# Optimization experiments

Hardware: AMD Instinct MI355X
Metric: run time of the kernel (lower is better)

The kernel has to match this reference:

```python
import jax, jax.numpy as jnp
import numpy as np

N = 100_000          # NEURON_COUNT (scaled)
INPUT_SIZE = 1024    # input neurons occupy indices [0, INPUT_SIZE)
OUTPUT_SIZE = 256    # output neurons occupy indices [N-OUTPUT_SIZE, N)
E = 10_000_000       # SYNAPSE_RATIO * N
STEPS = 3


def setup_inputs() -> dict:
    key = jax.random.key(0)
    k1, k2, k3, k4, k5 = jax.random.split(key, 5)
    x = jax.random.normal(k1, (INPUT_SIZE,), dtype=jnp.float32)
    synapse_weights = jax.random.normal(k2, (E,), dtype=jnp.float32)
    neuron_biases = jax.random.normal(k3, (N - INPUT_SIZE,), dtype=jnp.float32)
    synapse_src = jax.random.randint(k4, (E,), 0, N, dtype=jnp.int64) if jax.config.jax_enable_x64 else jax.random.randint(k4, (E,), 0, N, dtype=jnp.int32)
    synapse_dst = jax.random.randint(k5, (E,), 0, N, dtype=jnp.int64) if jax.config.jax_enable_x64 else jax.random.randint(k5, (E,), 0, N, dtype=jnp.int32)
    return {
        "x": x,
        "synapse_weights": synapse_weights,
        "neuron_biases": neuron_biases,
        "synapse_src": synapse_src,
        "synapse_dst": synapse_dst,
    }


def reference(x, synapse_weights, neuron_biases, synapse_src, synapse_dst):
    # Initial state: zeros everywhere, inputs injected at the first INPUT_SIZE slots.
    v = jnp.zeros((N,), dtype=x.dtype).at[:INPUT_SIZE].set(x.reshape(-1))
    # tanh applied to all neurons except outputs (last OUTPUT_SIZE indices)
    tanh_mask = jnp.arange(N) < (N - OUTPUT_SIZE)
    for _ in range(STEPS):
        # vectorized gather-multiply-scatter: next[to] += v[from] * w  (one segment_sum)
        msg = v[synapse_src] * synapse_weights                       # [E]
        nxt = jax.ops.segment_sum(msg, synapse_dst, num_segments=N)  # [N]
        # biases added to all non-input neurons
        nxt = nxt.at[INPUT_SIZE:].add(neuron_biases)
        # tanh everywhere except output neurons
        v = jnp.where(tanh_mask, jnp.tanh(nxt), nxt)
    return v[N - OUTPUT_SIZE:]
```

## Files before the change

### kernel.cpp

```cpp
#include <hip/hip_runtime.h>

#define N_NEURONS   100000
#define INPUT_SIZE  1024
#define OUTPUT_SIZE 256
#define E_SYN       10000000
#define STEPS       3

#define RANGES      8
#define BIN         12500
#define SCAT_BLK    512
#define CBLK        96
#define CAP         1280000
#define RB_BLK      256
#define CH          5000
#define B_CNT       2000
#define VEC4        (E_SYN / 4)

__global__ void init_all(const float* __restrict__ x, float* __restrict__ v,
                         int* __restrict__ gcur) {
    int i = blockIdx.x * blockDim.x + threadIdx.x;
    if (i < N_NEURONS) v[i] = (i < INPUT_SIZE) ? x[i] : 0.0f;
    if (i < RANGES) gcur[i] = 0;
}

__global__ void reorder_partition(const float* __restrict__ w,
                                  const int*   __restrict__ src,
                                  const int*   __restrict__ dst,
                                  int2* __restrict__ recs,
                                  int*  __restrict__ gcur) {
    __shared__ int cnt[RANGES];
    __shared__ int cursor[RANGES];
    const int tid  = threadIdx.x;
    const int lane = tid & 63;
    const unsigned long long ltmask = (1ull << lane) - 1ull;
    if (tid < RANGES) cnt[tid] = 0;
    __syncthreads();

    const int beg  = blockIdx.x * CH;
    const int endx = beg + CH;
    const int ITER = (CH + RB_BLK - 1) / RB_BLK;

    int wcnt = 0;
    for (int it = 0; it < ITER; ++it) {
        int  e  = beg + it * RB_BLK + tid;
        bool ok = (e < endx);
        int  r  = ok ? (dst[e] / BIN) : -1;
#pragma unroll
        for (int rr = 0; rr < RANGES; ++rr) {
            unsigned long long mask = __ballot(r == rr);
            if (lane == rr) wcnt += __popcll(mask);
        }
    }
    if (lane < RANGES) atomicAdd(&cnt[lane], wcnt);
    __syncthreads();
    if (tid < RANGES) cursor[tid] = tid * CAP + atomicAdd(&gcur[tid], cnt[tid]);
    __syncthreads();

    for (int it = 0; it < ITER; ++it) {
        int  e  = beg + it * RB_BLK + tid;
        bool ok = (e < endx);
        int  d  = ok ? dst[e] : 0;
        int  r  = ok ? (d / BIN) : -1;
        int  pos = 0;
#pragma unroll
        for (int rr = 0; rr < RANGES; ++rr) {
            unsigned long long mask = __ballot(r == rr);
            int tot = __popcll(mask);
            int b = 0;
            if (lane == rr) b = atomicAdd(&cursor[rr], tot);
            b = __shfl(b, rr, 64);
            if (r == rr) pos = b + __popcll(mask & ltmask);
        }
        if (ok) {
            int code = (src[e] << 14) | (d - r * BIN);
            recs[pos] = make_int2(code, __float_as_int(w[e]));
        }
    }
}

__global__ __launch_bounds__(SCAT_BLK) void scatter_sorted(
        const int2* __restrict__ recs,
        const int*  __restrict__ gcur,
        const float* __restrict__ v,
        float* __restrict__ partials) {
    __shared__ float bins[BIN];
    const int r = blockIdx.x / CBLK;
    const int c = blockIdx.x % CBLK;
    for (int j = threadIdx.x; j < BIN; j += SCAT_BLK) bins[j] = 0.0f;
    __syncthreads();

    const int cnt   = gcur[r];
    const int npair = cnt >> 1;
    const int4* base4 = (const int4*)(recs + (size_t)r * CAP);
    const int stride = CBLK * SCAT_BLK;
    for (int u = c * SCAT_BLK + threadIdx.x; u < npair; u += stride) {
        int4 p = base4[u];
        atomicAdd(&bins[p.x & 16383], v[p.x >> 14] * __int_as_float(p.y));
        atomicAdd(&bins[p.z & 16383], v[p.z >> 14] * __int_as_float(p.w));
    }
    if ((cnt & 1) && c == 0 && threadIdx.x == 0) {
        int2 p = recs[(size_t)r * CAP + cnt - 1];
        atomicAdd(&bins[p.x & 16383], v[p.x >> 14] * __int_as_float(p.y));
    }
    __syncthreads();
    float* o = partials + (size_t)(r * CBLK + c) * BIN;
    for (int j = threadIdx.x; j < BIN; j += SCAT_BLK) o[j] = bins[j];
}

__global__ void reduce_update(const float* __restrict__ partials,
                              const float* __restrict__ bias,
                              float* __restrict__ v,
                              float* __restrict__ out,
                              int C, int write_out) {
    int i4 = 4 * (blockIdx.x * blockDim.x + threadIdx.x);
    if (i4 >= N_NEURONS) return;
    const int r = i4 / BIN;
    const int j = i4 - r * BIN;
    const float* base = partials + ((size_t)r * C) * BIN + j;
    float4 acc = {0.f, 0.f, 0.f, 0.f};
    for (int c = 0; c < C; ++c) {
        float4 p = *(const float4*)(base + (size_t)c * BIN);
        acc.x += p.x; acc.y += p.y; acc.z += p.z; acc.w += p.w;
    }
    float av[4] = {acc.x, acc.y, acc.z, acc.w};
#pragma unroll
    for (int k = 0; k < 4; ++k) {
        int i = i4 + k;
        float val = av[k] + ((i >= INPUT_SIZE) ? bias[i - INPUT_SIZE] : 0.0f);
        float nv  = (i < N_NEURONS - OUTPUT_SIZE) ? tanhf(val) : val;
        v[i] = nv;
        if (write_out && i >= N_NEURONS - OUTPUT_SIZE)
            out[i - (N_NEURONS - OUTPUT_SIZE)] = val;
    }
}

__global__ void init_state_fb(const float* __restrict__ x, float* __restrict__ v) {
    int i = blockIdx.x * blockDim.x + threadIdx.x;
    if (i < N_NEURONS) v[i] = (i < INPUT_SIZE) ? x[i] : 0.0f;
}
__global__ void scatter_binned(const float* __restrict__ w,
                               const int*   __restrict__ src,
                               const int*   __restrict__ dst,
                               const float* __restrict__ v,
                               float*       __restrict__ partials,
                               int C) {
    __shared__ float bins[BIN];
    const int r = blockIdx.x / C;
    const int c = blockIdx.x % C;
    const int lo = r * BIN;
    const int hi = lo + BIN;
    for (int j = threadIdx.x; j < BIN; j += blockDim.x) bins[j] = 0.0f;
    __syncthreads();
    const int4*   src4 = (const int4*)src;
    const int4*   dst4 = (const int4*)dst;
    const float4* w4v  = (const float4*)w;
    const int stride = C * blockDim.x;
    for (int u = c * blockDim.x + threadIdx.x; u < VEC4; u += stride) {
        const int4   s4 = src4[u];
        const int4   d4 = dst4[u];
        const float4 wv = w4v[u];
        int   s[4] = {s4.x, s4.y, s4.z, s4.w};
        int   d[4] = {d4.x, d4.y, d4.z, d4.w};
        float ww[4] = {wv.x, wv.y, wv.z, wv.w};
#pragma unroll
        for (int k = 0; k < 4; ++k)
            if (d[k] >= lo && d[k] < hi)
                atomicAdd(&bins[d[k] - lo], v[s[k]] * ww[k]);
    }
    __syncthreads();
    float* o = partials + ((size_t)(r * C + c)) * BIN;
    for (int j = threadIdx.x; j < BIN; j += blockDim.x) o[j] = bins[j];
}

extern "C" void kernel_launch(void* const* d_in, const int* in_sizes, int n_in,
                              void* d_out, int out_size, void* d_ws, size_t ws_size,
                              hipStream_t stream) {
    const float* x    = (const float*)d_in[0];
    const float* w    = (const float*)d_in[1];
    const float* bias = (const float*)d_in[2];
    const int*   src  = (const int*)d_in[3];
    const int*   dst  = (const int*)d_in[4];
    float* out = (float*)d_out;

    const int blk = 256;
    const int grid_n   = (N_NEURONS + blk - 1) / blk;
    const int red_grid = (N_NEURONS / 4 + blk - 1) / blk;

    float* v        = (float*)d_ws;
    float* partials = v + N_NEURONS;
    int2*  recs     = (int2*)(partials + (size_t)RANGES * CBLK * BIN);
    int*   gcur     = (int*)(recs + (size_t)RANGES * CAP);
    size_t need = (size_t)((char*)(gcur + RANGES) - (char*)d_ws);

    if (ws_size >= need) {
        init_all<<<grid_n, blk, 0, stream>>>(x, v, gcur);
        reorder_partition<<<B_CNT, RB_BLK, 0, stream>>>(w, src, dst, recs, gcur);
        for (int s = 0; s < STEPS; ++s) {
            scatter_sorted<<<RANGES * CBLK, SCAT_BLK, 0, stream>>>(
                recs, gcur, v, partials);
            reduce_update<<<red_grid, blk, 0, stream>>>(
                partials, bias, v, out, CBLK, s == STEPS - 1 ? 1 : 0);
        }
    } else {
        long C = (long)(ws_size / 4 / N_NEURONS) - 1;
        if (C > 64) C = 64;
        if (C < 1) C = 1;
        float* part_fb = v + N_NEURONS;
        init_state_fb<<<grid_n, blk, 0, stream>>>(x, v);
        for (int s = 0; s < STEPS; ++s) {
            scatter_binned<<<RANGES * (int)C, SCAT_BLK, 0, stream>>>(
                w, src, dst, v, part_fb, (int)C);
            reduce_update<<<red_grid, blk, 0, stream>>>(
                part_fb, bias, v, out, (int)C, s == STEPS - 1 ? 1 : 0);
        }
    }
}
```

Measured before the change: 461.1 us.

## Speed up partition with ballot bit-planes, unroll scatter, split reduction into two stages

```diff
diff --git a/kernel.cpp b/kernel.cpp
--- a/kernel.cpp
+++ b/kernel.cpp
@@ -10,10 +10,12 @@
 #define BIN         12500
 #define SCAT_BLK    512
 #define CBLK        96
+#define RG          8
+#define RSL         (CBLK / RG)
 #define CAP         1280000
 #define RB_BLK      256
-#define CH          5000
-#define B_CNT       2000
+#define CH          4000
+#define B_CNT       2500
 #define VEC4        (E_SYN / 4)
 
 __global__ void init_all(const float* __restrict__ x, float* __restrict__ v,
@@ -23,15 +25,18 @@
     if (i < RANGES) gcur[i] = 0;
 }
 
-__global__ void reorder_partition(const float* __restrict__ w,
-                                  const int*   __restrict__ src,
-                                  const int*   __restrict__ dst,
-                                  int2* __restrict__ recs,
-                                  int*  __restrict__ gcur) {
+__global__ __launch_bounds__(RB_BLK) void reorder_partition(
+        const float* __restrict__ w,
+        const int*   __restrict__ src,
+        const int*   __restrict__ dst,
+        int2* __restrict__ recs,
+        int*  __restrict__ gcur) {
     __shared__ int cnt[RANGES];
     __shared__ int cursor[RANGES];
+    __shared__ int wbase[RB_BLK / 64][RANGES];
     const int tid  = threadIdx.x;
     const int lane = tid & 63;
+    const int wv   = tid >> 6;
     const unsigned long long ltmask = (1ull << lane) - 1ull;
     if (tid < RANGES) cnt[tid] = 0;
     __syncthreads();
@@ -39,42 +44,59 @@
     const int beg  = blockIdx.x * CH;
     const int endx = beg + CH;
     const int ITER = (CH + RB_BLK - 1) / RB_BLK;
-
-    int wcnt = 0;
-    for (int it = 0; it < ITER; ++it) {
-        int  e  = beg + it * RB_BLK + tid;
-        bool ok = (e < endx);
-        int  r  = ok ? (dst[e] / BIN) : -1;
-#pragma unroll
-        for (int rr = 0; rr < RANGES; ++rr) {
-            unsigned long long mask = __ballot(r == rr);
-            if (lane == rr) wcnt += __popcll(mask);
-        }
-    }
-    if (lane < RANGES) atomicAdd(&cnt[lane], wcnt);
-    __syncthreads();
-    if (tid < RANGES) cursor[tid] = tid * CAP + atomicAdd(&gcur[tid], cnt[tid]);
-    __syncthreads();
-
+    const int* wi  = (const int*)w;
+
+    int h[RANGES] = {0, 0, 0, 0, 0, 0, 0, 0};
     for (int it = 0; it < ITER; ++it) {
         int  e  = beg + it * RB_BLK + tid;
         bool ok = (e < endx);
         int  d  = ok ? dst[e] : 0;
-        int  r  = ok ? (d / BIN) : -1;
-        int  pos = 0;
+        int  r  = d / BIN;
+        unsigned long long okm = __ballot(ok);
+        unsigned long long b0  = __ballot(r & 1);
+        unsigned long long b1  = __ballot(r & 2);
+        unsigned long long b2  = __ballot(r & 4);
 #pragma unroll
         for (int rr = 0; rr < RANGES; ++rr) {
-            unsigned long long mask = __ballot(r == rr);
-            int tot = __popcll(mask);
-            int b = 0;
-            if (lane == rr) b = atomicAdd(&cursor[rr], tot);
-            b = __shfl(b, rr, 64);
-            if (r == rr) pos = b + __popcll(mask & ltmask);
+            unsigned long long m = ((rr & 1) ? b0 : ~b0) &
+                                   ((rr & 2) ? b1 : ~b1) &
+                                   ((rr & 4) ? b2 : ~b2) & okm;
+            h[rr] += __popcll(m);
         }
-        if (ok) {
-            int code = (src[e] << 14) | (d - r * BIN);
-            recs[pos] = make_int2(code, __float_as_int(w[e]));
-        }
+    }
+    if (lane < RANGES) {
+        int t = h[0];
+#pragma unroll
+        for (int rr = 1; rr < RANGES; ++rr) if (lane == rr) t = h[rr];
+        atomicAdd(&cnt[lane], t);
+    }
+    __syncthreads();
+    if (tid < RANGES) cursor[tid] = tid * CAP + atomicAdd(&gcur[tid], cnt[tid]);
+    __syncthreads();
+
+    for (int it = 0; it < ITER; ++it) {
+        int  e  = beg + it * RB_BLK + tid;
+        bool ok = (e < endx);
+        int  d  = ok ? dst[e] : 0;
+        int  sv = ok ? src[e] : 0;
+        int  wb = ok ? wi[e]  : 0;
+        int  r  = d / BIN;
+        unsigned long long okm = __ballot(ok);
+        unsigned long long b0  = __ballot(r & 1);
+        unsigned long long b1  = __ballot(r & 2);
+        unsigned long long b2  = __ballot(r & 4);
+        unsigned long long s0 = (lane & 1) ? b0 : ~b0;
+        unsigned long long s1 = (lane & 2) ? b1 : ~b1;
+        unsigned long long s2 = (lane & 4) ? b2 : ~b2;
+        int tot = __popcll(s0 & s1 & s2 & okm);
+        if (lane < RANGES) wbase[wv][lane] = atomicAdd(&cursor[lane], tot);
+        unsigned long long m0 = (r & 1) ? b0 : ~b0;
+        unsigned long long m1 = (r & 2) ? b1 : ~b1;
+        unsigned long long m2 = (r & 4) ? b2 : ~b2;
+        unsigned long long mym = m0 & m1 & m2 & okm;
+        int base = wbase[wv][r];
+        int pos  = base + __popcll(mym & ltmask);
+        if (ok) recs[pos] = make_int2((sv << 14) | (d - r * BIN), wb);
     }
 }
 
@@ -93,10 +115,23 @@
     const int npair = cnt >> 1;
     const int4* base4 = (const int4*)(recs + (size_t)r * CAP);
     const int stride = CBLK * SCAT_BLK;
-    for (int u = c * SCAT_BLK + threadIdx.x; u < npair; u += stride) {
-        int4 p = base4[u];
-        atomicAdd(&bins[p.x & 16383], v[p.x >> 14] * __int_as_float(p.y));
-        atomicAdd(&bins[p.z & 16383], v[p.z >> 14] * __int_as_float(p.w));
+    int u = c * SCAT_BLK + threadIdx.x;
+    for (; u + stride < npair; u += 2 * stride) {
+        int4 a = base4[u];
+        int4 b = base4[u + stride];
+        float va0 = v[a.x >> 14];
+        float va1 = v[a.z >> 14];
+        float vb0 = v[b.x >> 14];
+        float vb1 = v[b.z >> 14];
+        atomicAdd(&bins[a.x & 16383], va0 * __int_as_float(a.y));
+        atomicAdd(&bins[a.z & 16383], va1 * __int_as_float(a.w));
+        atomicAdd(&bins[b.x & 16383], vb0 * __int_as_float(b.y));
+        atomicAdd(&bins[b.z & 16383], vb1 * __int_as_float(b.w));
+    }
+    if (u < npair) {
+        int4 a = base4[u];
+        atomicAdd(&bins[a.x & 16383], v[a.x >> 14] * __int_as_float(a.y));
+        atomicAdd(&bins[a.z & 16383], v[a.z >> 14] * __int_as_float(a.w));
     }
     if ((cnt & 1) && c == 0 && threadIdx.x == 0) {
         int2 p = recs[(size_t)r * CAP + cnt - 1];
@@ -107,19 +142,34 @@
     for (int j = threadIdx.x; j < BIN; j += SCAT_BLK) o[j] = bins[j];
 }
 
-__global__ void reduce_update(const float* __restrict__ partials,
+__global__ void reduce_stage1(const float* __restrict__ partials,
+                              float* __restrict__ p2) {
+    int i4 = 4 * (blockIdx.x * blockDim.x + threadIdx.x);
+    if (i4 >= N_NEURONS) return;
+    const int g = blockIdx.y;
+    const int r = i4 / BIN;
+    const int j = i4 - r * BIN;
+    const float* base = partials + ((size_t)(r * CBLK + g * RSL)) * BIN + j;
+    float4 acc = {0.f, 0.f, 0.f, 0.f};
+#pragma unroll
+    for (int c = 0; c < RSL; ++c) {
+        float4 p = *(const float4*)(base + (size_t)c * BIN);
+        acc.x += p.x; acc.y += p.y; acc.z += p.z; acc.w += p.w;
+    }
+    *(float4*)(p2 + (size_t)g * N_NEURONS + i4) = acc;
+}
+
+__global__ void reduce_stage2(const float* __restrict__ p2,
                               const float* __restrict__ bias,
                               float* __restrict__ v,
                               float* __restrict__ out,
-                              int C, int write_out) {
+                              int write_out) {
     int i4 = 4 * (blockIdx.x * blockDim.x + threadIdx.x);
     if (i4 >= N_NEURONS) return;
-    const int r = i4 / BIN;
-    const int j = i4 - r * BIN;
-    const float* base = partials + ((size_t)r * C) * BIN + j;
     float4 acc = {0.f, 0.f, 0.f, 0.f};
-    for (int c = 0; c < C; ++c) {
-        float4 p = *(const float4*)(base + (size_t)c * BIN);
+#pragma unroll
+    for (int g = 0; g < RG; ++g) {
+        float4 p = *(const float4*)(p2 + (size_t)g * N_NEURONS + i4);
         acc.x += p.x; acc.y += p.y; acc.z += p.z; acc.w += p.w;
     }
     float av[4] = {acc.x, acc.y, acc.z, acc.w};
@@ -171,6 +221,32 @@
     float* o = partials + ((size_t)(r * C + c)) * BIN;
     for (int j = threadIdx.x; j < BIN; j += blockDim.x) o[j] = bins[j];
 }
+__global__ void reduce_update_fb(const float* __restrict__ partials,
+                                 const float* __restrict__ bias,
+                                 float* __restrict__ v,
+                                 float* __restrict__ out,
+                                 int C, int write_out) {
+    int i4 = 4 * (blockIdx.x * blockDim.x + threadIdx.x);
+    if (i4 >= N_NEURONS) return;
+    const int r = i4 / BIN;
+    const int j = i4 - r * BIN;
+    const float* base = partials + ((size_t)r * C) * BIN + j;
+    float4 acc = {0.f, 0.f, 0.f, 0.f};
+    for (int c = 0; c < C; ++c) {
+        float4 p = *(const float4*)(base + (size_t)c * BIN);
+        acc.x += p.x; acc.y += p.y; acc.z += p.z; acc.w += p.w;
+    }
+    float av[4] = {acc.x, acc.y, acc.z, acc.w};
+#pragma unroll
+    for (int k = 0; k < 4; ++k) {
+        int i = i4 + k;
+        float val = av[k] + ((i >= INPUT_SIZE) ? bias[i - INPUT_SIZE] : 0.0f);
+        float nv  = (i < N_NEURONS - OUTPUT_SIZE) ? tanhf(val) : val;
+        v[i] = nv;
+        if (write_out && i >= N_NEURONS - OUTPUT_SIZE)
+            out[i - (N_NEURONS - OUTPUT_SIZE)] = val;
+    }
+}
 
 extern "C" void kernel_launch(void* const* d_in, const int* in_sizes, int n_in,
                               void* d_out, int out_size, void* d_ws, size_t ws_size,
@@ -188,7 +264,8 @@
 
     float* v        = (float*)d_ws;
     float* partials = v + N_NEURONS;
-    int2*  recs     = (int2*)(partials + (size_t)RANGES * CBLK * BIN);
+    float* p2       = partials + (size_t)RANGES * CBLK * BIN;
+    int2*  recs     = (int2*)(p2 + (size_t)RG * N_NEURONS);
     int*   gcur     = (int*)(recs + (size_t)RANGES * CAP);
     size_t need = (size_t)((char*)(gcur + RANGES) - (char*)d_ws);
 
@@ -198,8 +275,9 @@
         for (int s = 0; s < STEPS; ++s) {
             scatter_sorted<<<RANGES * CBLK, SCAT_BLK, 0, stream>>>(
                 recs, gcur, v, partials);
-            reduce_update<<<red_grid, blk, 0, stream>>>(
-                partials, bias, v, out, CBLK, s == STEPS - 1 ? 1 : 0);
+            reduce_stage1<<<dim3(red_grid, RG), blk, 0, stream>>>(partials, p2);
+            reduce_stage2<<<red_grid, blk, 0, stream>>>(
+                p2, bias, v, out, s == STEPS - 1 ? 1 : 0);
         }
     } else {
         long C = (long)(ws_size / 4 / N_NEURONS) - 1;
@@ -210,7 +288,7 @@
         for (int s = 0; s < STEPS; ++s) {
             scatter_binned<<<RANGES * (int)C, SCAT_BLK, 0, stream>>>(
                 w, src, dst, v, part_fb, (int)C);
-            reduce_update<<<red_grid, blk, 0, stream>>>(
+            reduce_update_fb<<<red_grid, blk, 0, stream>>>(
                 part_fb, bias, v, out, (int)C, s == STEPS - 1 ? 1 : 0);
         }
     }
```

Result: faster. 420.3 us (-8.9%).
